# Performance work log

Measured on AMD Instinct MI355X. Metric: run time of the kernel, lower is better.

## Reference

```python
import jax, jax.numpy as jnp
import numpy as np

N_NODES = 50000
N_EDGES = 500000
IN_CH = 256
HID = 64
HEADS = 8
OUT_CH = 16
NEG_SLOPE = 0.2  # PyG GATConv default


def setup_inputs() -> dict:
    key = jax.random.key(0)
    ks = jax.random.split(key, 10)
    x = jax.random.normal(ks[0], (N_NODES, IN_CH), dtype=jnp.float32)
    edge_index = jax.random.randint(ks[1], (2, N_EDGES), 0, N_NODES, dtype=jnp.int64)
    s1 = 1.0 / np.sqrt(IN_CH)
    W1 = jax.random.uniform(ks[2], (IN_CH, HEADS * HID), jnp.float32, -s1, s1)
    att_src1 = jax.random.normal(ks[3], (HEADS, HID), dtype=jnp.float32) * 0.1
    att_dst1 = jax.random.normal(ks[4], (HEADS, HID), dtype=jnp.float32) * 0.1
    b1 = jnp.zeros((HEADS * HID,), jnp.float32)
    s2 = 1.0 / np.sqrt(HEADS * HID)
    W2 = jax.random.uniform(ks[5], (HEADS * HID, OUT_CH), jnp.float32, -s2, s2)
    att_src2 = jax.random.normal(ks[6], (1, OUT_CH), dtype=jnp.float32) * 0.1
    att_dst2 = jax.random.normal(ks[7], (1, OUT_CH), dtype=jnp.float32) * 0.1
    b2 = jnp.zeros((OUT_CH,), jnp.float32)
    return {"x": x, "edge_index": edge_index, "W1": W1, "att_src1": att_src1,
            "att_dst1": att_dst1, "b1": b1, "W2": W2, "att_src2": att_src2,
            "att_dst2": att_dst2, "b2": b2}


def _gat_conv(x, src, dst, W, att_src, att_dst, bias, heads, out_ch, concat, n_nodes):
    # Linear transform: [N, H, C]
    h = (x @ W).reshape(n_nodes, heads, out_ch)
    # Per-node attention logits: [N, H]
    a_src = jnp.einsum('nhc,hc->nh', h, att_src)
    a_dst = jnp.einsum('nhc,hc->nh', h, att_dst)
    # Edge-wise attention score (message src -> dst): [E, H]
    e = jax.nn.leaky_relu(a_src[src] + a_dst[dst], NEG_SLOPE)
    # Segment softmax over incoming edges of each destination node
    emax = jax.ops.segment_max(e, dst, num_segments=n_nodes)  # [N, H]
    emax = jnp.where(jnp.isfinite(emax), emax, 0.0)
    e = jnp.exp(e - emax[dst])
    denom = jax.ops.segment_sum(e, dst, num_segments=n_nodes)  # [N, H]
    alpha = e / (denom[dst] + 1e-16)
    # Weighted scatter-add aggregation: [N, H, C]
    msg = h[src] * alpha[:, :, None]
    out = jax.ops.segment_sum(msg, dst, num_segments=n_nodes)
    if concat:
        out = out.reshape(n_nodes, heads * out_ch)
    else:
        out = out.mean(axis=1)
    return out + bias


def reference(x, edge_index, W1, att_src1, att_dst1, b1, W2, att_src2, att_dst2, b2):
    n = x.shape[0]
    # PyG GATConv adds self-loops by default
    loops = jnp.arange(n, dtype=edge_index.dtype)
    src = jnp.concatenate([edge_index[0], loops])
    dst = jnp.concatenate([edge_index[1], loops])
    # dropout (p=0.6) is identity in eval mode
    h = _gat_conv(x, src, dst, W1, att_src1, att_dst1, b1, HEADS, HID, True, n)
    h = jax.nn.elu(h)
    out = _gat_conv(h, src, dst, W2, att_src2, att_dst2, b2, 1, OUT_CH, False, n)
    return jax.nn.log_softmax(out, axis=1)
```

## Files before the change

### kernel.cpp

```cpp
#include <hip/hip_runtime.h>
#include <math.h>

#define N_NODES 50000
#define N_EDGES 500000
#define IN_CH 256
#define D1 512
#define HEADS 8
#define HID 64
#define OUT_CH 16
#define NEG_SLOPE 0.2f

typedef __bf16 bf16x8 __attribute__((ext_vector_type(8)));
typedef float f32x4 __attribute__((ext_vector_type(4)));
typedef float f32x2 __attribute__((ext_vector_type(2)));

__device__ inline void fp8x8_to_f32(uint2 u, float* f) {
    f32x2 p0 = __builtin_amdgcn_cvt_pk_f32_fp8(u.x, false);
    f32x2 p1 = __builtin_amdgcn_cvt_pk_f32_fp8(u.x, true);
    f32x2 p2 = __builtin_amdgcn_cvt_pk_f32_fp8(u.y, false);
    f32x2 p3 = __builtin_amdgcn_cvt_pk_f32_fp8(u.y, true);
    f[0] = p0.x; f[1] = p0.y; f[2] = p1.x; f[3] = p1.y;
    f[4] = p2.x; f[5] = p2.y; f[6] = p3.x; f[7] = p3.y;
}

__device__ inline void fp8x16_to_f32(uint4 u, float* f) {
    fp8x8_to_f32(make_uint2(u.x, u.y), f);
    fp8x8_to_f32(make_uint2(u.z, u.w), f + 8);
}

__device__ inline unsigned char f32_to_fp8(float v) {
    return (unsigned char)(__builtin_amdgcn_cvt_pk_fp8_f32(v, v, 0, false) & 0xff);
}

__global__ __launch_bounds__(256) void k_prep(const float* __restrict__ W1,
                                              const float* __restrict__ W2,
                                              const int* __restrict__ edst,
                                              __bf16* __restrict__ Wt,
                                              __bf16* __restrict__ Wt2,
                                              int* __restrict__ deg) {
    int t = blockIdx.x * 256 + threadIdx.x;
    int nthr = gridDim.x * 256;
    for (int i = t; i < D1 * IN_CH; i += nthr) {
        int n = i >> 8, k = i & 255;
        Wt[i] = (__bf16)W1[k * D1 + n];
    }
    for (int i = t; i < D1 * OUT_CH; i += nthr) {
        int n = i >> 9, k = i & 511;
        Wt2[i] = (__bf16)W2[k * OUT_CH + n];
    }
    for (int i = t; i < N_EDGES; i += nthr) atomicAdd(&deg[edst[i]], 1);
}

__global__ __launch_bounds__(256) void k_gemm1_mfma(const float* __restrict__ X,
                                                    const __bf16* __restrict__ Wt,
                                                    const float* __restrict__ att_src,
                                                    const float* __restrict__ att_dst,
                                                    unsigned char* __restrict__ Hf8,
                                                    float* __restrict__ a_src1,
                                                    float* __restrict__ a_dst1) {
    __shared__ __bf16 As[128][40];
    __shared__ __bf16 Bs[128][40];
    int tid = threadIdx.x;
    int wid = tid >> 6, lane = tid & 63;
    int wr = wid >> 1, wc = wid & 1;
    int row0 = blockIdx.x * 128;
    int col0 = blockIdx.y * 128;
    int lq = lane >> 4;
    int lm = lane & 15;
    f32x4 acc[4][4] = {};
    for (int k0 = 0; k0 < IN_CH; k0 += 32) {
        #pragma unroll
        for (int it = 0; it < 2; ++it) {
            int idx = tid + it * 256;
            int r  = idx >> 2;
            int c8 = (idx & 3) * 8;
            int gr = row0 + r;
            __bf16 ob[8];
            if (gr < N_NODES) {
                const float* xp = &X[(size_t)gr * IN_CH + k0 + c8];
                float4 v0 = *(const float4*)xp;
                float4 v1 = *(const float4*)(xp + 4);
                ob[0] = (__bf16)v0.x; ob[1] = (__bf16)v0.y;
                ob[2] = (__bf16)v0.z; ob[3] = (__bf16)v0.w;
                ob[4] = (__bf16)v1.x; ob[5] = (__bf16)v1.y;
                ob[6] = (__bf16)v1.z; ob[7] = (__bf16)v1.w;
            } else {
                #pragma unroll
                for (int j = 0; j < 8; ++j) ob[j] = (__bf16)0.f;
            }
            *(uint4*)&As[r][c8] = *(uint4*)ob;
            uint4 vb = *(const uint4*)&Wt[(size_t)(col0 + r) * IN_CH + k0 + c8];
            *(uint4*)&Bs[r][c8] = vb;
        }
        __syncthreads();
        bf16x8 af[4], bfr[4];
        #pragma unroll
        for (int i = 0; i < 4; ++i) af[i]  = *(bf16x8*)&As[wr * 64 + i * 16 + lm][lq * 8];
        #pragma unroll
        for (int j = 0; j < 4; ++j) bfr[j] = *(bf16x8*)&Bs[wc * 64 + j * 16 + lm][lq * 8];
        #pragma unroll
        for (int i = 0; i < 4; ++i)
            #pragma unroll
            for (int j = 0; j < 4; ++j)
                acc[i][j] = __builtin_amdgcn_mfma_f32_16x16x32_bf16(af[i], bfr[j], acc[i][j], 0, 0, 0);
        __syncthreads();
    }
    int head = blockIdx.y * 2 + wc;
    float as_v[4], ad_v[4];
    #pragma unroll
    for (int j = 0; j < 4; ++j) {
        as_v[j] = att_src[head * HID + j * 16 + lm];
        ad_v[j] = att_dst[head * HID + j * 16 + lm];
    }
    #pragma unroll
    for (int i = 0; i < 4; ++i) {
        int rbase = row0 + wr * 64 + i * 16 + lq * 4;
        #pragma unroll
        for (int r = 0; r < 4; ++r) {
            int grow = rbase + r;
            float ps = 0.f, pd = 0.f;
            #pragma unroll
            for (int j = 0; j < 4; ++j) {
                float v = acc[i][j][r];
                ps += v * as_v[j];
                pd += v * ad_v[j];
                if (grow < N_NODES)
                    Hf8[(size_t)grow * D1 + col0 + wc * 64 + j * 16 + lm] = f32_to_fp8(v);
            }
            #pragma unroll
            for (int off = 1; off < 16; off <<= 1) {
                ps += __shfl_xor(ps, off);
                pd += __shfl_xor(pd, off);
            }
            if (lm == 0 && grow < N_NODES) {
                a_src1[grow * HEADS + head] = ps;
                a_dst1[grow * HEADS + head] = pd;
            }
        }
    }
}

__global__ __launch_bounds__(1024) void k_scan1(const int* __restrict__ deg,
                                                int* __restrict__ offsets,
                                                int* __restrict__ bsum) {
    __shared__ int wsum[16];
    int tid = threadIdx.x, lane = tid & 63, wid = tid >> 6;
    int i = blockIdx.x * 1024 + tid;
    int v = (i < N_NODES) ? deg[i] : 0;
    int x = v;
    #pragma unroll
    for (int off = 1; off < 64; off <<= 1) {
        int t = __shfl_up(x, off);
        if (lane >= off) x += t;
    }
    if (lane == 63) wsum[wid] = x;
    __syncthreads();
    if (wid == 0) {
        int s = (lane < 16) ? wsum[lane] : 0;
        #pragma unroll
        for (int off = 1; off < 16; off <<= 1) {
            int t = __shfl_up(s, off);
            if (lane >= off) s += t;
        }
        if (lane < 16) wsum[lane] = s;
    }
    __syncthreads();
    int wbase = wid ? wsum[wid - 1] : 0;
    if (i < N_NODES) offsets[i] = wbase + x - v;
    if (tid == 1023) bsum[blockIdx.x] = wsum[15];
}

__global__ __launch_bounds__(256) void k_scan3(int* __restrict__ offsets,
                                               const int* __restrict__ bsum,
                                               int* __restrict__ cursor) {
    __shared__ int bpre_s[64];
    int tid = threadIdx.x;
    const int nb = (N_NODES + 1023) / 1024;
    if (tid < 64) {
        int v = (tid < nb) ? bsum[tid] : 0;
        int x = v;
        #pragma unroll
        for (int off = 1; off < 64; off <<= 1) {
            int t = __shfl_up(x, off);
            if (tid >= off) x += t;
        }
        bpre_s[tid] = x - v;
        if (blockIdx.x == 0 && tid == nb - 1) offsets[N_NODES] = x;
    }
    __syncthreads();
    int i = blockIdx.x * 256 + tid;
    if (i < N_NODES) {
        int o = offsets[i] + bpre_s[i >> 10];
        offsets[i] = o;
        cursor[i] = o;
    }
}

__global__ void k_scatter(const int* __restrict__ esrc, const int* __restrict__ edst,
                          const float* __restrict__ a_src, const float* __restrict__ a_dst,
                          int* __restrict__ cursor, int* __restrict__ csr,
                          float* __restrict__ w1) {
    int e = blockIdx.x * blockDim.x + threadIdx.x;
    if (e >= N_EDGES) return;
    int s = esrc[e], d = edst[e];
    int pos = atomicAdd(&cursor[d], 1);
    csr[pos] = s;
    float4 s0 = *(const float4*)&a_src[s * HEADS];
    float4 s1 = *(const float4*)&a_src[s * HEADS + 4];
    float4 d0 = *(const float4*)&a_dst[d * HEADS];
    float4 d1 = *(const float4*)&a_dst[d * HEADS + 4];
    float ev[8] = {s0.x + d0.x, s0.y + d0.y, s0.z + d0.z, s0.w + d0.w,
                   s1.x + d1.x, s1.y + d1.y, s1.z + d1.z, s1.w + d1.w};
    float w[8];
    #pragma unroll
    for (int h = 0; h < 8; ++h) {
        float v = ev[h] > 0.f ? ev[h] : NEG_SLOPE * ev[h];
        w[h] = __expf(v);
    }
    *(float4*)&w1[(size_t)pos * 8]     = make_float4(w[0], w[1], w[2], w[3]);
    *(float4*)&w1[(size_t)pos * 8 + 4] = make_float4(w[4], w[5], w[6], w[7]);
}

__global__ __launch_bounds__(256) void k_agg1(const unsigned char* __restrict__ Hf8,
                                              const float* __restrict__ a_src,
                                              const float* __restrict__ a_dst,
                                              const float* __restrict__ w1,
                                              const int* __restrict__ offsets,
                                              const int* __restrict__ csr,
                                              const float* __restrict__ b1,
                                              __bf16* __restrict__ OUT) {
    int wave = (blockIdx.x * blockDim.x + threadIdx.x) >> 6;
    int lane = threadIdx.x & 63;
    if (wave >= N_NODES) return;
    int d = wave;
    int half = lane >> 5;
    int l32 = lane & 31;
    int chb = l32 * 16;
    int head = l32 >> 2;
    float o[16];
    #pragma unroll
    for (int j = 0; j < 16; ++j) o[j] = 0.f;
    float lsum = 0.f;
    if (half == 0) {
        float es = a_src[d * HEADS + head] + a_dst[d * HEADS + head];
        es = es > 0.f ? es : NEG_SLOPE * es;
        float wself = __expf(es);
        uint4 hu = *(const uint4*)&Hf8[(size_t)d * D1 + chb];
        float hv[16];
        fp8x16_to_f32(hu, hv);
        lsum = wself;
        #pragma unroll
        for (int j = 0; j < 16; ++j) o[j] = wself * hv[j];
    }
    int beg = offsets[d], end = offsets[d + 1];
    int idx = beg;
    for (; idx + 4 <= end; idx += 4) {
        int eA = idx + half, eB = idx + 2 + half;
        int sA = csr[eA], sB = csr[eB];
        float wA = w1[(size_t)eA * 8 + head];
        float wB = w1[(size_t)eB * 8 + head];
        uint4 uA = *(const uint4*)&Hf8[(size_t)sA * D1 + chb];
        uint4 uB = *(const uint4*)&Hf8[(size_t)sB * D1 + chb];
        float fA[16], fB[16];
        fp8x16_to_f32(uA, fA);
        fp8x16_to_f32(uB, fB);
        lsum += wA + wB;
        #pragma unroll
        for (int j = 0; j < 16; ++j) o[j] += wA * fA[j] + wB * fB[j];
    }
    for (; idx < end; idx += 2) {
        int e = idx + half;
        bool valid = e < end;
        int s = valid ? csr[e] : csr[idx];
        float w = valid ? w1[(size_t)e * 8 + head] : 0.f;
        uint4 u = *(const uint4*)&Hf8[(size_t)s * D1 + chb];
        float f[16];
        fp8x16_to_f32(u, f);
        lsum += w;
        #pragma unroll
        for (int j = 0; j < 16; ++j) o[j] += w * f[j];
    }
    #pragma unroll
    for (int j = 0; j < 16; ++j) o[j] += __shfl_xor(o[j], 32);
    lsum += __shfl_xor(lsum, 32);
    if (half == 0) {
        float inv = 1.0f / (lsum + 1e-16f);
        __bf16 r[16];
        #pragma unroll
        for (int j = 0; j < 16; ++j) {
            float v = o[j] * inv + b1[chb + j];
            v = v > 0.f ? v : (__expf(v) - 1.0f);
            r[j] = (__bf16)v;
        }
        *(uint4*)&OUT[(size_t)d * D1 + chb]     = *(uint4*)&r[0];
        *(uint4*)&OUT[(size_t)d * D1 + chb + 8] = *(uint4*)&r[8];
    }
}

__global__ __launch_bounds__(256) void k_gemm2_mfma(const __bf16* __restrict__ A,
                                                    const __bf16* __restrict__ Wt2,
                                                    const float* __restrict__ as2v,
                                                    const float* __restrict__ ad2v,
                                                    __bf16* __restrict__ H2,
                                                    float* __restrict__ a_src2,
                                                    float* __restrict__ a_dst2) {
    int tid = threadIdx.x;
    int wid = tid >> 6, lane = tid & 63;
    int lq = lane >> 4, lm = lane & 15;
    int row0 = blockIdx.x * 64 + wid * 16;
    int arow = row0 + lm;
    const __bf16* ap = A + (size_t)(arow < N_NODES ? arow : 0) * D1;
    f32x4 acc = {};
    #pragma unroll
    for (int k0 = 0; k0 < 16; ++k0) {
        bf16x8 af  = *(const bf16x8*)&ap[k0 * 32 + lq * 8];
        bf16x8 bfr = *(const bf16x8*)&Wt2[lm * D1 + k0 * 32 + lq * 8];
        acc = __builtin_amdgcn_mfma_f32_16x16x32_bf16(af, bfr, acc, 0, 0, 0);
    }
    float as_c = as2v[lm], ad_c = ad2v[lm];
    #pragma unroll
    for (int r = 0; r < 4; ++r) {
        int gr = row0 + lq * 4 + r;
        float v = acc[r];
        if (gr < N_NODES) H2[gr * OUT_CH + lm] = (__bf16)v;
        float ps = v * as_c, pd = v * ad_c;
        #pragma unroll
        for (int off = 1; off < 16; off <<= 1) {
            ps += __shfl_xor(ps, off);
            pd += __shfl_xor(pd, off);
        }
        if (lm == 0 && gr < N_NODES) { a_src2[gr] = ps; a_dst2[gr] = pd; }
    }
}

__global__ __launch_bounds__(256) void k_agg2(const __bf16* __restrict__ H2,
                                              const float* __restrict__ a_src,
                                              const float* __restrict__ a_dst,
                                              const int* __restrict__ offsets,
                                              const int* __restrict__ csr,
                                              const float* __restrict__ b2,
                                              float* __restrict__ OUT) {
    int wave = (blockIdx.x * blockDim.x + threadIdx.x) >> 6;
    int lane = threadIdx.x & 63;
    if (wave >= N_NODES) return;
    int d = wave;
    int g = lane >> 4, c = lane & 15;
    float ad = a_dst[d];
    float es = a_src[d] + ad;
    es = es > 0.f ? es : NEG_SLOPE * es;
    float wself = __expf(es);
    int beg = offsets[d], end = offsets[d + 1];
    float o = 0.f, lsum = 0.f;
    if (g == 0) {
        o = wself * (float)H2[d * OUT_CH + c];
        lsum = wself;
    }
    for (int idx = beg + g; idx < end; idx += 4) {
        int s = csr[idx];
        float e = a_src[s] + ad;
        e = e > 0.f ? e : NEG_SLOPE * e;
        float w = __expf(e);
        lsum += w;
        o += w * (float)H2[s * OUT_CH + c];
    }
    o += __shfl_xor(o, 16);  o += __shfl_xor(o, 32);
    lsum += __shfl_xor(lsum, 16);  lsum += __shfl_xor(lsum, 32);
    float v = o / (lsum + 1e-16f) + b2[c];
    float mx = v;
    #pragma unroll
    for (int off = 1; off < 16; off <<= 1) mx = fmaxf(mx, __shfl_xor(mx, off));
    float se = __expf(v - mx);
    #pragma unroll
    for (int off = 1; off < 16; off <<= 1) se += __shfl_xor(se, off);
    float res = v - mx - logf(se);
    if (lane < 16) OUT[d * OUT_CH + lane] = res;
}

extern "C" void kernel_launch(void* const* d_in, const int* in_sizes, int n_in,
                              void* d_out, int out_size, void* d_ws, size_t ws_size,
                              hipStream_t stream) {
    const float* x        = (const float*)d_in[0];
    const int*   ei       = (const int*)d_in[1];
    const float* W1       = (const float*)d_in[2];
    const float* att_src1 = (const float*)d_in[3];
    const float* att_dst1 = (const float*)d_in[4];
    const float* b1       = (const float*)d_in[5];
    const float* W2       = (const float*)d_in[6];
    const float* att_src2 = (const float*)d_in[7];
    const float* att_dst2 = (const float*)d_in[8];
    const float* b2       = (const float*)d_in[9];
    float* out = (float*)d_out;

    const int* esrc = ei;
    const int* edst = ei + N_EDGES;

    char* ws = (char*)d_ws;
    size_t off = 0;
    auto alloc = [&](size_t bytes) { char* p = ws + off; off = (off + bytes + 255) & ~(size_t)255; return p; };
    unsigned char* Hf8 = (unsigned char*)alloc((size_t)N_NODES * D1);
    __bf16* out1   = (__bf16*)alloc((size_t)N_NODES * D1 * 2);
    __bf16* Wt     = (__bf16*)alloc((size_t)D1 * IN_CH * 2);
    __bf16* Wt2    = (__bf16*)alloc((size_t)D1 * OUT_CH * 2);
    float* a_src1  = (float*)alloc((size_t)N_NODES * HEADS * 4);
    float* a_dst1  = (float*)alloc((size_t)N_NODES * HEADS * 4);
    float* w1      = (float*)alloc((size_t)N_EDGES * HEADS * 4);
    __bf16* h2     = (__bf16*)alloc((size_t)N_NODES * OUT_CH * 2);
    float* a_src2  = (float*)alloc((size_t)N_NODES * 4);
    float* a_dst2  = (float*)alloc((size_t)N_NODES * 4);
    int*   deg     = (int*)alloc((size_t)N_NODES * 4);
    int*   offsets = (int*)alloc((size_t)(N_NODES + 1) * 4);
    int*   cursor  = (int*)alloc((size_t)N_NODES * 4);
    int*   csr     = (int*)alloc((size_t)N_EDGES * 4);
    int*   bsum    = (int*)alloc(64 * 4);
    (void)ws_size;

    hipMemsetAsync(deg, 0, (size_t)N_NODES * 4, stream);
    k_prep<<<512, 256, 0, stream>>>(W1, W2, edst, Wt, Wt2, deg);
    dim3 g1((N_NODES + 127) / 128, D1 / 128);
    k_gemm1_mfma<<<g1, 256, 0, stream>>>(x, Wt, att_src1, att_dst1, Hf8, a_src1, a_dst1);
    int nb = (N_NODES + 1023) / 1024;
    k_scan1<<<nb, 1024, 0, stream>>>(deg, offsets, bsum);
    k_scan3<<<(N_NODES + 255) / 256, 256, 0, stream>>>(offsets, bsum, cursor);
    k_scatter<<<(N_EDGES + 255) / 256, 256, 0, stream>>>(esrc, edst, a_src1, a_dst1,
                                                         cursor, csr, w1);
    k_agg1<<<(N_NODES * 64 + 255) / 256, 256, 0, stream>>>(Hf8, a_src1, a_dst1, w1, offsets, csr, b1, out1);
    k_gemm2_mfma<<<(N_NODES + 63) / 64, 256, 0, stream>>>(out1, Wt2, att_src2, att_dst2, h2, a_src2, a_dst2);
    k_agg2<<<(N_NODES * 64 + 255) / 256, 256, 0, stream>>>(h2, a_src2, a_dst2, offsets, csr, b2, out);
}
```

Baseline: 304.6 us.

## Pre-convert X to bf16 in prep and register-prefetch next K tile in GEMM1

Moves the fp32-to-bf16 conversion of X out of the GEMM1 inner loop into the prep kernel, which writes a bf16 copy of X. GEMM1 then loads bf16 tiles directly and prefetches the next K tile into registers while the MFMAs for the current tile run. This halves the bytes GEMM1 reads from X across its four column blocks and hides load latency. In exchange it adds a full extra pass over X plus a 25 MB bf16 write in prep, a larger workspace, and an extra barrier per K step.

```diff
diff --git a/kernel.cpp b/kernel.cpp
--- a/kernel.cpp
+++ b/kernel.cpp
@@ -32,14 +32,24 @@
     return (unsigned char)(__builtin_amdgcn_cvt_pk_fp8_f32(v, v, 0, false) & 0xff);
 }
 
-__global__ __launch_bounds__(256) void k_prep(const float* __restrict__ W1,
+__global__ __launch_bounds__(256) void k_prep(const float* __restrict__ X,
+                                              const float* __restrict__ W1,
                                               const float* __restrict__ W2,
                                               const int* __restrict__ edst,
+                                              __bf16* __restrict__ Xb,
                                               __bf16* __restrict__ Wt,
                                               __bf16* __restrict__ Wt2,
                                               int* __restrict__ deg) {
     int t = blockIdx.x * 256 + threadIdx.x;
     int nthr = gridDim.x * 256;
+    for (int i = t; i < N_NODES * IN_CH / 8; i += nthr) {
+        size_t base = (size_t)i * 8;
+        float4 v0 = *(const float4*)&X[base];
+        float4 v1 = *(const float4*)&X[base + 4];
+        __bf16 o[8] = {(__bf16)v0.x, (__bf16)v0.y, (__bf16)v0.z, (__bf16)v0.w,
+                       (__bf16)v1.x, (__bf16)v1.y, (__bf16)v1.z, (__bf16)v1.w};
+        *(uint4*)&Xb[base] = *(uint4*)o;
+    }
     for (int i = t; i < D1 * IN_CH; i += nthr) {
         int n = i >> 8, k = i & 255;
         Wt[i] = (__bf16)W1[k * D1 + n];
@@ -51,7 +61,7 @@
     for (int i = t; i < N_EDGES; i += nthr) atomicAdd(&deg[edst[i]], 1);
 }
 
-__global__ __launch_bounds__(256) void k_gemm1_mfma(const float* __restrict__ X,
+__global__ __launch_bounds__(256) void k_gemm1_mfma(const __bf16* __restrict__ Xb,
                                                     const __bf16* __restrict__ Wt,
                                                     const float* __restrict__ att_src,
                                                     const float* __restrict__ att_dst,
@@ -67,32 +77,39 @@
     int col0 = blockIdx.y * 128;
     int lq = lane >> 4;
     int lm = lane & 15;
+    int r_st[2], c_st[2];
+    #pragma unroll
+    for (int it = 0; it < 2; ++it) {
+        int idx = tid + it * 256;
+        r_st[it] = idx >> 2;
+        c_st[it] = (idx & 3) * 8;
+    }
     f32x4 acc[4][4] = {};
-    for (int k0 = 0; k0 < IN_CH; k0 += 32) {
-        #pragma unroll
-        for (int it = 0; it < 2; ++it) {
-            int idx = tid + it * 256;
-            int r  = idx >> 2;
-            int c8 = (idx & 3) * 8;
-            int gr = row0 + r;
-            __bf16 ob[8];
-            if (gr < N_NODES) {
-                const float* xp = &X[(size_t)gr * IN_CH + k0 + c8];
-                float4 v0 = *(const float4*)xp;
-                float4 v1 = *(const float4*)(xp + 4);
-                ob[0] = (__bf16)v0.x; ob[1] = (__bf16)v0.y;
-                ob[2] = (__bf16)v0.z; ob[3] = (__bf16)v0.w;
-                ob[4] = (__bf16)v1.x; ob[5] = (__bf16)v1.y;
-                ob[6] = (__bf16)v1.z; ob[7] = (__bf16)v1.w;
-            } else {
-                #pragma unroll
-                for (int j = 0; j < 8; ++j) ob[j] = (__bf16)0.f;
+    uint4 pa[2], pb[2];
+    #pragma unroll
+    for (int it = 0; it < 2; ++it) {
+        int gr = row0 + r_st[it];
+        pa[it] = (gr < N_NODES) ? *(const uint4*)&Xb[(size_t)gr * IN_CH + c_st[it]]
+                                : make_uint4(0u, 0u, 0u, 0u);
+        pb[it] = *(const uint4*)&Wt[(size_t)(col0 + r_st[it]) * IN_CH + c_st[it]];
+    }
+    #pragma unroll
+    for (int it = 0; it < 2; ++it) {
+        *(uint4*)&As[r_st[it]][c_st[it]] = pa[it];
+        *(uint4*)&Bs[r_st[it]][c_st[it]] = pb[it];
+    }
+    __syncthreads();
+    for (int kt = 0; kt < IN_CH / 32; ++kt) {
+        if (kt + 1 < IN_CH / 32) {
+            int k0 = (kt + 1) * 32;
+            #pragma unroll
+            for (int it = 0; it < 2; ++it) {
+                int gr = row0 + r_st[it];
+                pa[it] = (gr < N_NODES) ? *(const uint4*)&Xb[(size_t)gr * IN_CH + k0 + c_st[it]]
+                                        : make_uint4(0u, 0u, 0u, 0u);
+                pb[it] = *(const uint4*)&Wt[(size_t)(col0 + r_st[it]) * IN_CH + k0 + c_st[it]];
             }
-            *(uint4*)&As[r][c8] = *(uint4*)ob;
-            uint4 vb = *(const uint4*)&Wt[(size_t)(col0 + r) * IN_CH + k0 + c8];
-            *(uint4*)&Bs[r][c8] = vb;
-        }
-        __syncthreads();
+        }
         bf16x8 af[4], bfr[4];
         #pragma unroll
         for (int i = 0; i < 4; ++i) af[i]  = *(bf16x8*)&As[wr * 64 + i * 16 + lm][lq * 8];
@@ -103,7 +120,15 @@
             #pragma unroll
             for (int j = 0; j < 4; ++j)
                 acc[i][j] = __builtin_amdgcn_mfma_f32_16x16x32_bf16(af[i], bfr[j], acc[i][j], 0, 0, 0);
-        __syncthreads();
+        if (kt + 1 < IN_CH / 32) {
+            __syncthreads();
+            #pragma unroll
+            for (int it = 0; it < 2; ++it) {
+                *(uint4*)&As[r_st[it]][c_st[it]] = pa[it];
+                *(uint4*)&Bs[r_st[it]][c_st[it]] = pb[it];
+            }
+            __syncthreads();
+        }
     }
     int head = blockIdx.y * 2 + wc;
     float as_v[4], ad_v[4];
@@ -399,6 +424,7 @@
     auto alloc = [&](size_t bytes) { char* p = ws + off; off = (off + bytes + 255) & ~(size_t)255; return p; };
     unsigned char* Hf8 = (unsigned char*)alloc((size_t)N_NODES * D1);
     __bf16* out1   = (__bf16*)alloc((size_t)N_NODES * D1 * 2);
+    __bf16* Xb     = (__bf16*)alloc((size_t)N_NODES * IN_CH * 2);
     __bf16* Wt     = (__bf16*)alloc((size_t)D1 * IN_CH * 2);
     __bf16* Wt2    = (__bf16*)alloc((size_t)D1 * OUT_CH * 2);
     float* a_src1  = (float*)alloc((size_t)N_NODES * HEADS * 4);
@@ -415,9 +441,9 @@
     (void)ws_size;
 
     hipMemsetAsync(deg, 0, (size_t)N_NODES * 4, stream);
-    k_prep<<<512, 256, 0, stream>>>(W1, W2, edst, Wt, Wt2, deg);
+    k_prep<<<512, 256, 0, stream>>>(x, W1, W2, edst, Xb, Wt, Wt2, deg);
     dim3 g1((N_NODES + 127) / 128, D1 / 128);
-    k_gemm1_mfma<<<g1, 256, 0, stream>>>(x, Wt, att_src1, att_dst1, Hf8, a_src1, a_dst1);
+    k_gemm1_mfma<<<g1, 256, 0, stream>>>(Xb, Wt, att_src1, att_dst1, Hf8, a_src1, a_dst1);
     int nb = (N_NODES + 1023) / 1024;
     k_scan1<<<nb, 1024, 0, stream>>>(deg, offsets, bsum);
     k_scan3<<<(N_NODES + 255) / 256, 256, 0, stream>>>(offsets, bsum, cursor);
```

Measured after the change: 319.4 us. 1.05x slower.
